# Performance work log

Measured on AMD Instinct MI355X. Metric: run time of the kernel, lower is better.

The kernel has to match this reference:

```python
import jax, jax.numpy as jnp
import numpy as np


def setup_inputs() -> dict:
    key = jax.random.key(0)
    k1, k2 = jax.random.split(key)
    x = jax.random.normal(k1, (32, 128, 128, 128), dtype=jnp.float32)
    conv_w = jax.random.normal(k2, (1, 2, 7, 7), dtype=jnp.float32) * 0.1
    return {"x": x, "conv_w": conv_w}


def reference(x, conv_w):
    # x: [B, C, H, W]; conv_w: [1, 2, 7, 7]
    max_out = jnp.max(x, axis=1, keepdims=True)   # [B,1,H,W]
    avg_out = jnp.mean(x, axis=1, keepdims=True)  # [B,1,H,W]
    stacked = jnp.concatenate([avg_out, max_out], axis=1)  # [B,2,H,W]
    attn = jax.lax.conv_general_dilated(
        stacked, conv_w,
        window_strides=(1, 1), padding=((3, 3), (3, 3)),
        dimension_numbers=("NCHW", "OIHW", "NCHW"),
    )  # [B,1,H,W]
    return x * jax.nn.sigmoid(attn)
```

## Files before the change

kernel.cpp:

```cpp
#include <hip/hip_runtime.h>

#define BB 32
#define CC 128
#define HH 128
#define WW 128
#define HWSZ (HH * WW)
#define CHW (CC * HWSZ)
#define S4 (HWSZ / 4)
#define RPB 8
#define HALO 14

typedef float vfloat4 __attribute__((ext_vector_type(4)));

__device__ __forceinline__ vfloat4 fmax4(vfloat4 a, vfloat4 b) {
    vfloat4 r;
    r.x = fmaxf(a.x, b.x);
    r.y = fmaxf(a.y, b.y);
    r.z = fmaxf(a.z, b.z);
    r.w = fmaxf(a.w, b.w);
    return r;
}

__global__ __launch_bounds__(256, 2) void sa_onepass(
    const float* __restrict__ x, const float* __restrict__ cw,
    float* __restrict__ out) {
    __shared__ float m_lds[2][HALO][WW];
    __shared__ float wsh[2 * 49];

    const int tid = threadIdx.x;
    const int wg  = blockIdx.x;
    const int xcd = wg & 7;
    const int lin = wg >> 3;
    const int b   = xcd * 4 + (lin >> 4);
    const int hb  = lin & 15;
    const int h0  = hb * RPB;

    if (tid < 98) wsh[tid] = cw[tid];

    const int r0 = tid >> 5;
    const int w4 = tid & 31;
    const float* xb = x + (size_t)b * CHW;

    const bool actB = (r0 < HALO - 8);
    const int gh_a = h0 - 3 + r0;
    const int gh_b = h0 - 3 + r0 + 8;
    const bool okA = (gh_a >= 0) && (gh_a < HH);
    const bool okB = actB && (gh_b < HH);
    const int cha = gh_a < 0 ? 0 : (gh_a > HH - 1 ? HH - 1 : gh_a);
    const int chb = gh_b > HH - 1 ? HH - 1 : gh_b;

    const vfloat4* pA = (const vfloat4*)(xb + cha * WW) + w4;
    const vfloat4* pB = (const vfloat4*)(xb + chb * WW) + w4;

    vfloat4 sumA, mxA;
    {
        vfloat4 v = pA[0];
        sumA = v; mxA = v;
    }
    #pragma unroll 4
    for (int c = 1; c < CC; ++c) {
        vfloat4 v = pA[(size_t)c * S4];
        sumA += v;
        mxA = fmax4(mxA, v);
    }
    vfloat4 sumB = {0.f, 0.f, 0.f, 0.f}, mxB = sumB;
    if (actB) {
        vfloat4 v = pB[0];
        sumB = v; mxB = v;
        #pragma unroll 4
        for (int c = 1; c < CC; ++c) {
            vfloat4 t = pB[(size_t)c * S4];
            sumB += t;
            mxB = fmax4(mxB, t);
        }
    }

    const float invC = 1.0f / (float)CC;
    {
        vfloat4 avgA = sumA * invC;
        if (!okA) { avgA = (vfloat4){0,0,0,0}; mxA = (vfloat4){0,0,0,0}; }
        *(vfloat4*)&m_lds[0][r0][w4 * 4] = avgA;
        *(vfloat4*)&m_lds[1][r0][w4 * 4] = mxA;
        if (actB) {
            vfloat4 avgB = sumB * invC;
            if (!okB) { avgB = (vfloat4){0,0,0,0}; mxB = (vfloat4){0,0,0,0}; }
            *(vfloat4*)&m_lds[0][r0 + 8][w4 * 4] = avgB;
            *(vfloat4*)&m_lds[1][r0 + 8][w4 * 4] = mxB;
        }
    }
    __syncthreads();

    const int hr = r0;
    const int w0 = w4 * 4;
    float attn[4] = {0.f, 0.f, 0.f, 0.f};
    #pragma unroll
    for (int ic = 0; ic < 2; ++ic) {
        #pragma unroll
        for (int kh = 0; kh < 7; ++kh) {
            const float* row = &m_lds[ic][hr + kh][0];
            float seg[10];
            #pragma unroll
            for (int k = 0; k < 10; ++k) {
                int wi = w0 - 3 + k;
                seg[k] = (wi >= 0 && wi < WW) ? row[wi] : 0.0f;
            }
            #pragma unroll
            for (int kw = 0; kw < 7; ++kw) {
                float wgt = wsh[ic * 49 + kh * 7 + kw];
                attn[0] = fmaf(seg[kw + 0], wgt, attn[0]);
                attn[1] = fmaf(seg[kw + 1], wgt, attn[1]);
                attn[2] = fmaf(seg[kw + 2], wgt, attn[2]);
                attn[3] = fmaf(seg[kw + 3], wgt, attn[3]);
            }
        }
    }
    vfloat4 sig;
    sig.x = 1.0f / (1.0f + __expf(-attn[0]));
    sig.y = 1.0f / (1.0f + __expf(-attn[1]));
    sig.z = 1.0f / (1.0f + __expf(-attn[2]));
    sig.w = 1.0f / (1.0f + __expf(-attn[3]));

    const int s = (h0 + hr) * WW + w0;
    const vfloat4* px = (const vfloat4*)xb + (s >> 2);
    vfloat4* po = (vfloat4*)(out + (size_t)b * CHW) + (s >> 2);
    #pragma unroll 4
    for (int c = CC - 1; c >= 0; --c) {
        vfloat4 v = px[(size_t)c * S4];
        v *= sig;
        __builtin_nontemporal_store(v, po + (size_t)c * S4);
    }
}

extern "C" void kernel_launch(void* const* d_in, const int* in_sizes, int n_in,
                              void* d_out, int out_size, void* d_ws, size_t ws_size,
                              hipStream_t stream) {
    const float* x  = (const float*)d_in[0];
    const float* cw = (const float*)d_in[1];
    float* out = (float*)d_out;

    sa_onepass<<<BB * (HH / RPB), 256, 0, stream>>>(x, cw, out);
}
```

Baseline: 141.3 us.

## Shrink row band per block to two rows and split channels across threads

Each block now handles 2 output rows instead of 8, launching four times as many blocks with higher occupancy bounds. The conv is computed one pixel per thread with sigmoid staged through shared memory, and the final scaling pass splits channels into four groups across threads. The aim is more parallelism and latency hiding. In exchange, the halo overhead grows from 14/8 to 8/2 rows re-read per block, adding redundant input traffic that must be absorbed by caches.

```diff
diff --git a/kernel.cpp b/kernel.cpp
--- a/kernel.cpp
+++ b/kernel.cpp
@@ -7,8 +7,9 @@
 #define HWSZ (HH * WW)
 #define CHW (CC * HWSZ)
 #define S4 (HWSZ / 4)
-#define RPB 8
-#define HALO 14
+#define RPB 2
+#define HALO 8
+#define NBAND (HH / RPB)
 
 typedef float vfloat4 __attribute__((ext_vector_type(4)));
 
@@ -21,113 +22,85 @@
     return r;
 }
 
-__global__ __launch_bounds__(256, 2) void sa_onepass(
+__global__ __launch_bounds__(256, 4) void sa_onepass(
     const float* __restrict__ x, const float* __restrict__ cw,
     float* __restrict__ out) {
     __shared__ float m_lds[2][HALO][WW];
+    __shared__ float sig_lds[RPB][WW];
     __shared__ float wsh[2 * 49];
 
     const int tid = threadIdx.x;
     const int wg  = blockIdx.x;
     const int xcd = wg & 7;
     const int lin = wg >> 3;
-    const int b   = xcd * 4 + (lin >> 4);
-    const int hb  = lin & 15;
+    const int b   = xcd * 4 + (lin >> 6);
+    const int hb  = lin & 63;
     const int h0  = hb * RPB;
 
     if (tid < 98) wsh[tid] = cw[tid];
 
-    const int r0 = tid >> 5;
-    const int w4 = tid & 31;
     const float* xb = x + (size_t)b * CHW;
 
-    const bool actB = (r0 < HALO - 8);
-    const int gh_a = h0 - 3 + r0;
-    const int gh_b = h0 - 3 + r0 + 8;
-    const bool okA = (gh_a >= 0) && (gh_a < HH);
-    const bool okB = actB && (gh_b < HH);
-    const int cha = gh_a < 0 ? 0 : (gh_a > HH - 1 ? HH - 1 : gh_a);
-    const int chb = gh_b > HH - 1 ? HH - 1 : gh_b;
-
-    const vfloat4* pA = (const vfloat4*)(xb + cha * WW) + w4;
-    const vfloat4* pB = (const vfloat4*)(xb + chb * WW) + w4;
-
-    vfloat4 sumA, mxA;
     {
-        vfloat4 v = pA[0];
-        sumA = v; mxA = v;
-    }
-    #pragma unroll 4
-    for (int c = 1; c < CC; ++c) {
-        vfloat4 v = pA[(size_t)c * S4];
-        sumA += v;
-        mxA = fmax4(mxA, v);
-    }
-    vfloat4 sumB = {0.f, 0.f, 0.f, 0.f}, mxB = sumB;
-    if (actB) {
-        vfloat4 v = pB[0];
-        sumB = v; mxB = v;
-        #pragma unroll 4
-        for (int c = 1; c < CC; ++c) {
-            vfloat4 t = pB[(size_t)c * S4];
-            sumB += t;
-            mxB = fmax4(mxB, t);
+        const int r  = tid >> 5;
+        const int w4 = tid & 31;
+        const int gh = h0 - 3 + r;
+        const bool ok = (gh >= 0) && (gh < HH);
+        vfloat4 sum = {0.f, 0.f, 0.f, 0.f}, mx = sum;
+        if (ok) {
+            const vfloat4* p = (const vfloat4*)(xb + gh * WW) + w4;
+            vfloat4 v = p[0];
+            sum = v; mx = v;
+            #pragma unroll 8
+            for (int c = 1; c < CC; ++c) {
+                vfloat4 t = p[(size_t)c * S4];
+                sum += t;
+                mx = fmax4(mx, t);
+            }
         }
-    }
-
-    const float invC = 1.0f / (float)CC;
-    {
-        vfloat4 avgA = sumA * invC;
-        if (!okA) { avgA = (vfloat4){0,0,0,0}; mxA = (vfloat4){0,0,0,0}; }
-        *(vfloat4*)&m_lds[0][r0][w4 * 4] = avgA;
-        *(vfloat4*)&m_lds[1][r0][w4 * 4] = mxA;
-        if (actB) {
-            vfloat4 avgB = sumB * invC;
-            if (!okB) { avgB = (vfloat4){0,0,0,0}; mxB = (vfloat4){0,0,0,0}; }
-            *(vfloat4*)&m_lds[0][r0 + 8][w4 * 4] = avgB;
-            *(vfloat4*)&m_lds[1][r0 + 8][w4 * 4] = mxB;
-        }
+        const float invC = 1.0f / (float)CC;
+        vfloat4 avg = sum * invC;
+        *(vfloat4*)&m_lds[0][r][w4 * 4] = avg;
+        *(vfloat4*)&m_lds[1][r][w4 * 4] = mx;
     }
     __syncthreads();
 
-    const int hr = r0;
-    const int w0 = w4 * 4;
-    float attn[4] = {0.f, 0.f, 0.f, 0.f};
-    #pragma unroll
-    for (int ic = 0; ic < 2; ++ic) {
+    {
+        const int hr = tid >> 7;
+        const int w  = tid & 127;
+        float attn = 0.f;
         #pragma unroll
-        for (int kh = 0; kh < 7; ++kh) {
-            const float* row = &m_lds[ic][hr + kh][0];
-            float seg[10];
+        for (int ic = 0; ic < 2; ++ic) {
             #pragma unroll
-            for (int k = 0; k < 10; ++k) {
-                int wi = w0 - 3 + k;
-                seg[k] = (wi >= 0 && wi < WW) ? row[wi] : 0.0f;
-            }
-            #pragma unroll
-            for (int kw = 0; kw < 7; ++kw) {
-                float wgt = wsh[ic * 49 + kh * 7 + kw];
-                attn[0] = fmaf(seg[kw + 0], wgt, attn[0]);
-                attn[1] = fmaf(seg[kw + 1], wgt, attn[1]);
-                attn[2] = fmaf(seg[kw + 2], wgt, attn[2]);
-                attn[3] = fmaf(seg[kw + 3], wgt, attn[3]);
+            for (int kh = 0; kh < 7; ++kh) {
+                const float* row = &m_lds[ic][hr + kh][0];
+                #pragma unroll
+                for (int kw = 0; kw < 7; ++kw) {
+                    int wi = w - 3 + kw;
+                    float v = (wi >= 0 && wi < WW) ? row[wi] : 0.0f;
+                    attn = fmaf(v, wsh[ic * 49 + kh * 7 + kw], attn);
+                }
             }
         }
+        sig_lds[hr][w] = 1.0f / (1.0f + __expf(-attn));
     }
-    vfloat4 sig;
-    sig.x = 1.0f / (1.0f + __expf(-attn[0]));
-    sig.y = 1.0f / (1.0f + __expf(-attn[1]));
-    sig.z = 1.0f / (1.0f + __expf(-attn[2]));
-    sig.w = 1.0f / (1.0f + __expf(-attn[3]));
+    __syncthreads();
 
-    const int s = (h0 + hr) * WW + w0;
-    const vfloat4* px = (const vfloat4*)xb + (s >> 2);
-    vfloat4* po = (vfloat4*)(out + (size_t)b * CHW) + (s >> 2);
-    #pragma unroll 4
-    for (int c = CC - 1; c >= 0; --c) {
-        vfloat4 v = px[(size_t)c * S4];
-        v *= sig;
-        __builtin_nontemporal_store(v, po + (size_t)c * S4);
+    {
+        const int cg = tid >> 6;
+        const int pos = tid & 63;
+        const int hr = pos >> 5;
+        const int w4 = pos & 31;
+        vfloat4 sig = *(const vfloat4*)&sig_lds[hr][w4 * 4];
+        const int s = (h0 + hr) * WW + w4 * 4;
+        const vfloat4* px = (const vfloat4*)xb + (s >> 2);
+        vfloat4* po = (vfloat4*)(out + (size_t)b * CHW) + (s >> 2);
+        #pragma unroll 4
+        for (int c = cg * 32; c < cg * 32 + 32; ++c) {
+            vfloat4 v = px[(size_t)c * S4];
+            v *= sig;
+            __builtin_nontemporal_store(v, po + (size_t)c * S4);
+        }
     }
 }
 
@@ -138,5 +111,5 @@
     const float* cw = (const float*)d_in[1];
     float* out = (float*)d_out;
 
-    sa_onepass<<<BB * (HH / RPB), 256, 0, stream>>>(x, cw, out);
+    sa_onepass<<<BB * NBAND, 256, 0, stream>>>(x, cw, out);
 }
```

Measured after the change: 206.2 us. 45.9% more time.
